# Kernel tuning notes

Hardware: AMD Instinct MI355X
Metric: run time of the kernel (lower is better)

The kernel has to match this reference:

```python
import jax, jax.numpy as jnp
import numpy as np

QMAX = 127.0  # 2**(bits-1) - 1 for bits=8, signed symmetric


def _quantize_signed_symmetric(t):
    # per-tensor symmetric: scale = max|t| / qmax, q = clamp(round(t/scale))
    scale = jnp.max(jnp.abs(t)) / QMAX
    q = jnp.clip(jnp.round(t / scale), -QMAX, QMAX)
    return q, scale


def setup_inputs() -> dict:
    key = jax.random.key(0)
    k1, k2, k3 = jax.random.split(key, 3)
    N, D_IN, D_OUT = 16384, 1024, 1024
    x = jax.random.normal(k1, (N, D_IN), dtype=jnp.float32)
    weight = jax.random.normal(k2, (D_OUT, D_IN), dtype=jnp.float32) * 0.02
    bias = jax.random.normal(k3, (D_OUT,), dtype=jnp.float32) * 0.01
    return {"x": x, "weight": weight, "bias": bias}


def reference(x, weight, bias):
    # weight quantization (cached in torch; recomputed here, same math)
    qw, w_scale = _quantize_signed_symmetric(weight)
    qw_t = qw.astype(jnp.int32).T            # [D_IN, D_OUT]
    # activation quantization
    qx, x_scale = _quantize_signed_symmetric(x)
    qx = qx.astype(jnp.int32)                # [N, D_IN]
    # int32 matmul, then per-tensor dequant + bias
    acc = qx @ qw_t                          # int32 [N, D_OUT]
    y = acc.astype(jnp.float32) * (x_scale * w_scale)
    return y + bias
```

## Files before the change

kernel.cpp:

```cpp
#include <hip/hip_runtime.h>

#define QMAX 127.0f

typedef int int4v __attribute__((ext_vector_type(4)));
typedef float float4v __attribute__((ext_vector_type(4)));

__device__ __forceinline__ float amax4(float4 v) {
    return fmaxf(fmaxf(fabsf(v.x), fabsf(v.y)), fmaxf(fabsf(v.z), fabsf(v.w)));
}
__device__ __forceinline__ int qone(float v, float s) {
    float q = fminf(fmaxf(rintf(v / s), -QMAX), QMAX);
    return (int)q;
}
__device__ __forceinline__ int qpack4(float4 v, float s) {
    return (qone(v.x, s) & 255) | ((qone(v.y, s) & 255) << 8) |
           ((qone(v.z, s) & 255) << 16) | ((qone(v.w, s) & 255) << 24);
}

__global__ void absmax2_kernel(const float4* __restrict__ px, int n4x,
                               const float4* __restrict__ pw, int n4w,
                               int gx, int* __restrict__ amax) {
    const float4* p; int n4; int* out; int nb, bid;
    if ((int)blockIdx.x < gx) { p = px; n4 = n4x; out = amax + 0; nb = gx; bid = blockIdx.x; }
    else { p = pw; n4 = n4w; out = amax + 1; nb = gridDim.x - gx; bid = blockIdx.x - gx; }
    const int S = nb * blockDim.x;
    int i = bid * blockDim.x + threadIdx.x;
    float a = 0.f, b = 0.f, c = 0.f, d = 0.f;
    for (; i + 3 * S < n4; i += 4 * S) {
        float4 v0 = p[i];
        float4 v1 = p[i + S];
        float4 v2 = p[i + 2 * S];
        float4 v3 = p[i + 3 * S];
        a = fmaxf(a, amax4(v0));
        b = fmaxf(b, amax4(v1));
        c = fmaxf(c, amax4(v2));
        d = fmaxf(d, amax4(v3));
    }
    for (; i < n4; i += S) a = fmaxf(a, amax4(p[i]));
    float m = fmaxf(fmaxf(a, b), fmaxf(c, d));
    for (int off = 32; off; off >>= 1) m = fmaxf(m, __shfl_down(m, off, 64));
    __shared__ float sm[4];
    if ((threadIdx.x & 63) == 0) sm[threadIdx.x >> 6] = m;
    __syncthreads();
    if (threadIdx.x == 0) {
        float bm = fmaxf(fmaxf(sm[0], sm[1]), fmaxf(sm[2], sm[3]));
        atomicMax(out, (int)__float_as_uint(bm));
    }
}

__global__ void quantw_kernel(const float4* __restrict__ sw, int4v* __restrict__ dw,
                              int n16w, int kshift, int KC,
                              const int* __restrict__ amax) {
    const float scale = __uint_as_float((unsigned)amax[1]) / QMAX;
    const int stride = gridDim.x * blockDim.x;
    for (int i = blockIdx.x * blockDim.x + threadIdx.x; i < n16w; i += stride) {
        float4 v0 = sw[4 * i + 0];
        float4 v1 = sw[4 * i + 1];
        float4 v2 = sw[4 * i + 2];
        float4 v3 = sw[4 * i + 3];
        int4v o = { qpack4(v0, scale), qpack4(v1, scale),
                    qpack4(v2, scale), qpack4(v3, scale) };
        const int n = i >> kshift;
        const int kg = i & ((1 << kshift) - 1);
        const int kc = kg >> 2, q = kg & 3;
        const int g = n >> 4, r = n & 15;
        dw[(g * KC + kc) * 64 + q * 16 + r] = o;
    }
}

__global__ __launch_bounds__(512, 2) void gemm_i8_kernel(
        const float* __restrict__ x, const char* __restrict__ qb,
        const float4* __restrict__ bias4, const int* __restrict__ amax,
        float* __restrict__ out, int M, int N, int K) {
    extern __shared__ char sA[];

    const int KC = K >> 6;
    const int NCH = KC >> 1;
    const int tid = threadIdx.x;
    const int lane = tid & 63;
    const int wv = tid >> 6;
    const int m0 = blockIdx.x * 64;

    const int si = wv >> 1;
    const int skcl = wv & 1;
    const int srow = m0 + si * 16 + (lane & 15);
    const int sk0 = skcl * 64 + (lane >> 4) * 16;
    const float4* sbase4 = (const float4*)(x + (size_t)srow * K + sk0);
    const int sslot = si * 128 + skcl * 64 + lane;

    const float xs = __uint_as_float((unsigned)amax[0]) / QMAX;

    const char* bbase = qb + (size_t)(wv * 8) * KC * 1024 + lane * 16;

#define LOADB(Bb, kc)                                                        \
    do { _Pragma("unroll") for (int j = 0; j < 8; ++j)                       \
        Bb[j] = *(const int4v*)(bbase + ((size_t)j * KC + (kc)) * 1024);     \
    } while (0)
#define LOADA(Af, buf, kcl)                                                  \
    do { const int4v* sAv = (const int4v*)(sA + (buf) * 8192);               \
        _Pragma("unroll") for (int i = 0; i < 4; ++i)                        \
            Af[i] = sAv[i * 128 + (kcl) * 64 + lane];                        \
    } while (0)
#define MF(Bb, Af)                                                           \
    do { _Pragma("unroll") for (int j = 0; j < 8; ++j)                       \
        _Pragma("unroll") for (int i = 0; i < 4; ++i)                        \
            acc[j][i] = __builtin_amdgcn_mfma_i32_16x16x64_i8(               \
                Bb[j], Af[i], acc[j][i], 0, 0, 0);                           \
    } while (0)
#define ISSUEA(h) do { xr0 = sbase4[(h) * 32]; xr1 = sbase4[(h) * 32 + 1]; } while (0)
#define ISSUEB(h) do { xr0 = sbase4[(h) * 32 + 2]; xr1 = sbase4[(h) * 32 + 3]; } while (0)

    float4 xr0, xr1;
    int qa0, qa1;
    int4v B0[8], B1[8], Af[4];

    ISSUEA(0);
    LOADB(B0, 0);
    qa0 = qpack4(xr0, xs); qa1 = qpack4(xr1, xs);
    ISSUEB(0);
    {
        int4v o = { qa0, qa1, qpack4(xr0, xs), qpack4(xr1, xs) };
        ((int4v*)sA)[sslot] = o;
    }
    __syncthreads();

    int4v acc[8][4];
    const int4v zero = {0, 0, 0, 0};
#pragma unroll
    for (int j = 0; j < 8; ++j)
#pragma unroll
        for (int i = 0; i < 4; ++i) acc[j][i] = zero;

#pragma unroll 1
    for (int h = 0; h < NCH - 1; ++h) {
        const int kc0 = h * 2;
        ISSUEA(h + 1);
        LOADB(B1, kc0 + 1);
        LOADA(Af, h & 1, 0);
        MF(B0, Af);
        qa0 = qpack4(xr0, xs); qa1 = qpack4(xr1, xs);
        ISSUEB(h + 1);
        LOADB(B0, kc0 + 2);
        LOADA(Af, h & 1, 1);
        MF(B1, Af);
        {
            int4v o = { qa0, qa1, qpack4(xr0, xs), qpack4(xr1, xs) };
            ((int4v*)(sA + ((h + 1) & 1) * 8192))[sslot] = o;
        }
        __syncthreads();
    }
    {
        const int kc0 = (NCH - 1) * 2;
        LOADB(B1, kc0 + 1);
        LOADA(Af, (NCH - 1) & 1, 0);
        MF(B0, Af);
        LOADA(Af, (NCH - 1) & 1, 1);
        MF(B1, Af);
    }

    const float sc = xs * (__uint_as_float((unsigned)amax[1]) / QMAX);
    const int quad = lane >> 4;
    const int rbase = m0 + (lane & 15);
    const int cb4 = wv * 32;
#pragma unroll
    for (int j = 0; j < 8; ++j) {
        const float4 bv = bias4[cb4 + j * 4 + quad];
#pragma unroll
        for (int i = 0; i < 4; ++i) {
            const int row = rbase + i * 16;
            float4v v;
            v[0] = (float)acc[j][i][0] * sc + bv.x;
            v[1] = (float)acc[j][i][1] * sc + bv.y;
            v[2] = (float)acc[j][i][2] * sc + bv.z;
            v[3] = (float)acc[j][i][3] * sc + bv.w;
            *((float4v*)(out + (size_t)row * N) + cb4 + j * 4 + quad) = v;
        }
    }
}

extern "C" void kernel_launch(void* const* d_in, const int* in_sizes, int n_in,
                              void* d_out, int out_size, void* d_ws, size_t ws_size,
                              hipStream_t stream) {
    const float* x = (const float*)d_in[0];
    const float* w = (const float*)d_in[1];
    const float* bias = (const float*)d_in[2];
    float* out = (float*)d_out;

    const int xn = in_sizes[0];
    const int wn = in_sizes[1];
    const int N = in_sizes[2];
    const int K = wn / N;
    const int M = xn / K;
    const int KC = K >> 6;
    const int kshift = __builtin_ctz(K >> 4);

    int* amax = (int*)d_ws;
    char* qw = (char*)d_ws + 1024;

    const int GAX = 2048, GAW = 256;
    absmax2_kernel<<<GAX + GAW, 256, 0, stream>>>(
        (const float4*)x, xn / 4, (const float4*)w, wn / 4, GAX, amax);

    quantw_kernel<<<256, 256, 0, stream>>>(
        (const float4*)w, (int4v*)qw, wn / 16, kshift, KC, amax);

    gemm_i8_kernel<<<M / 64, 512, 16384, stream>>>(
        x, qw, (const float4*)bias, amax, out, M, N, K);
}
```

Measured before the change: 178.5 us.

## Stage activation tiles via direct global-to-LDS loads with XOR swizzle

Replaces the per-thread register loads of fp32 activations with global_load_lds async copies into a swizzled 32KB LDS staging buffer. Quantization then reads from LDS and writes packed int8 into the double-buffered A area. The goal is to free registers and let the copies overlap with MFMA work without waiting on vector registers. It adds an extra barrier per iteration and triples LDS use to 48KB, which may reduce occupancy.

```diff
diff --git a/kernel.cpp b/kernel.cpp
--- a/kernel.cpp
+++ b/kernel.cpp
@@ -81,14 +81,13 @@
     const int wv = tid >> 6;
     const int m0 = blockIdx.x * 64;
 
-    const int si = wv >> 1;
-    const int skcl = wv & 1;
-    const int srow = m0 + si * 16 + (lane & 15);
-    const int sk0 = skcl * 64 + (lane >> 4) * 16;
-    const float4* sbase4 = (const float4*)(x + (size_t)srow * K + sk0);
-    const int sslot = si * 128 + skcl * 64 + lane;
-
     const float xs = __uint_as_float((unsigned)amax[0]) / QMAX;
+
+    const int r_ = lane & 15, q_ = lane >> 4;
+    const int i_ = tid >> 7, kcl_ = (tid >> 6) & 1;
+    const int qrow = i_ * 16 + r_;
+    const int cb = kcl_ * 16 + q_ * 4;
+    const int rx = qrow & 7;
 
     const char* bbase = qb + (size_t)(wv * 8) * KC * 1024 + lane * 16;
 
@@ -97,7 +96,7 @@
         Bb[j] = *(const int4v*)(bbase + ((size_t)j * KC + (kc)) * 1024);     \
     } while (0)
 #define LOADA(Af, buf, kcl)                                                  \
-    do { const int4v* sAv = (const int4v*)(sA + (buf) * 8192);               \
+    do { const int4v* sAv = (const int4v*)(sA + 32768 + (buf) * 8192);       \
         _Pragma("unroll") for (int i = 0; i < 4; ++i)                        \
             Af[i] = sAv[i * 128 + (kcl) * 64 + lane];                        \
     } while (0)
@@ -107,21 +106,36 @@
             acc[j][i] = __builtin_amdgcn_mfma_i32_16x16x64_i8(               \
                 Bb[j], Af[i], acc[j][i], 0, 0, 0);                           \
     } while (0)
-#define ISSUEA(h) do { xr0 = sbase4[(h) * 32]; xr1 = sbase4[(h) * 32 + 1]; } while (0)
-#define ISSUEB(h) do { xr0 = sbase4[(h) * 32 + 2]; xr1 = sbase4[(h) * 32 + 3]; } while (0)
-
-    float4 xr0, xr1;
-    int qa0, qa1;
+#define GSTAGE(h)                                                            \
+    do { _Pragma("unroll") for (int t = 0; t < 4; ++t) {                     \
+        const int R0 = wv * 8 + t * 2;                                       \
+        const int row = R0 + (lane >> 5);                                    \
+        const int cs = (lane & 31) ^ (row & 7);                              \
+        const char* src = (const char*)(x + (size_t)(m0 + row) * K           \
+                              + (h) * 128 + cs * 4);                         \
+        gload16(src, sA + (size_t)R0 * 512 + lane * 16);                     \
+    } } while (0)
+#define QUANT(pb)                                                            \
+    do { const float4* f4 = (const float4*)sA;                               \
+        float4 v0 = f4[qrow * 32 + ((cb + 0) ^ rx)];                         \
+        float4 v1 = f4[qrow * 32 + ((cb + 1) ^ rx)];                         \
+        float4 v2 = f4[qrow * 32 + ((cb + 2) ^ rx)];                         \
+        float4 v3 = f4[qrow * 32 + ((cb + 3) ^ rx)];                         \
+        int4v o = { qpack4(v0, xs), qpack4(v1, xs),                          \
+                    qpack4(v2, xs), qpack4(v3, xs) };                        \
+        ((int4v*)(sA + 32768 + (pb) * 8192))[tid] = o;                       \
+    } while (0)
+
+    typedef const __attribute__((address_space(1))) char glob_char;
+    typedef __attribute__((address_space(3))) char lds_char;
+#define gload16(g, l) __builtin_amdgcn_global_load_lds((glob_char*)(g), (lds_char*)(l), 16, 0, 0)
+
     int4v B0[8], B1[8], Af[4];
 
-    ISSUEA(0);
     LOADB(B0, 0);
-    qa0 = qpack4(xr0, xs); qa1 = qpack4(xr1, xs);
-    ISSUEB(0);
-    {
-        int4v o = { qa0, qa1, qpack4(xr0, xs), qpack4(xr1, xs) };
-        ((int4v*)sA)[sslot] = o;
-    }
+    GSTAGE(0);
+    __syncthreads();
+    QUANT(0);
     __syncthreads();
 
     int4v acc[8][4];
@@ -134,19 +148,15 @@
 #pragma unroll 1
     for (int h = 0; h < NCH - 1; ++h) {
         const int kc0 = h * 2;
-        ISSUEA(h + 1);
         LOADB(B1, kc0 + 1);
+        GSTAGE(h + 1);
         LOADA(Af, h & 1, 0);
         MF(B0, Af);
-        qa0 = qpack4(xr0, xs); qa1 = qpack4(xr1, xs);
-        ISSUEB(h + 1);
         LOADB(B0, kc0 + 2);
         LOADA(Af, h & 1, 1);
         MF(B1, Af);
-        {
-            int4v o = { qa0, qa1, qpack4(xr0, xs), qpack4(xr1, xs) };
-            ((int4v*)(sA + ((h + 1) & 1) * 8192))[sslot] = o;
-        }
+        __syncthreads();
+        QUANT((h + 1) & 1);
         __syncthreads();
     }
     {
@@ -204,6 +214,6 @@
     quantw_kernel<<<256, 256, 0, stream>>>(
         (const float4*)w, (int4v*)qw, wn / 16, kshift, KC, amax);
 
-    gemm_i8_kernel<<<M / 64, 512, 16384, stream>>>(
+    gemm_i8_kernel<<<M / 64, 512, 49152, stream>>>(
         x, qw, (const float4*)bias, amax, out, M, N, K);
 }
```

Result: faster. 170.1 us (-4.7%).
